# Performance work log

Measured on AMD Instinct MI355X. Metric: run time of the kernel, lower is better.

Reference implementation:

```python
import jax, jax.numpy as jnp
import numpy as np

H = 16  # hidden size

def _lstm_scan(xproj, Whh, bhh, collect_outputs):
    # xproj: [T, B, 4H] = input projection (W_ih @ x + b_ih), PyTorch gate order i,f,g,o
    B = xproj.shape[1]
    h0 = jnp.zeros((B, H), xproj.dtype)
    c0 = jnp.zeros((B, H), xproj.dtype)

    def step(carry, xt):
        h, c = carry
        g = xt + h @ Whh.T + bhh                      # [B, 4H]
        i, f, gg, o = jnp.split(g, 4, axis=-1)
        i = jax.nn.sigmoid(i)
        f = jax.nn.sigmoid(f)
        gg = jnp.tanh(gg)
        o = jax.nn.sigmoid(o)
        c = f * c + i * gg
        h = o * jnp.tanh(c)
        return (h, c), (h if collect_outputs else None)

    (hT, cT), hs = jax.lax.scan(step, (h0, c0), xproj)
    return hT, hs  # hs: [T, B, H] or None


def setup_inputs() -> dict:
    key = jax.random.key(0)
    ks = jax.random.split(key, 12)
    B, T = 4096, 1024
    s = 1.0 / np.sqrt(H)  # PyTorch LSTM init scale
    inp = {
        "x": jax.random.normal(ks[0], (B, T, 1), jnp.float32),
        "Wih0": jax.random.uniform(ks[1], (4 * H, 1), jnp.float32, -s, s),
        "Whh0": jax.random.uniform(ks[2], (4 * H, H), jnp.float32, -s, s),
        "bih0": jax.random.uniform(ks[3], (4 * H,), jnp.float32, -s, s),
        "bhh0": jax.random.uniform(ks[4], (4 * H,), jnp.float32, -s, s),
        "Wih1": jax.random.uniform(ks[5], (4 * H, H), jnp.float32, -s, s),
        "Whh1": jax.random.uniform(ks[6], (4 * H, H), jnp.float32, -s, s),
        "bih1": jax.random.uniform(ks[7], (4 * H,), jnp.float32, -s, s),
        "bhh1": jax.random.uniform(ks[8], (4 * H,), jnp.float32, -s, s),
        "Wout": jax.random.uniform(ks[9], (5, H), jnp.float32, -s, s),
        "bout": jax.random.uniform(ks[10], (5,), jnp.float32, -s, s),
    }
    return inp


def reference(x, Wih0, Whh0, bih0, bhh0, Wih1, Whh1, bih1, bhh1, Wout, bout):
    # Layer 1: precompute input projection for all timesteps, scan recurrence.
    # x: [B, T, 1] -> [T, B, 4H]
    xp0 = jnp.transpose(x @ Wih0.T + bih0, (1, 0, 2))
    _, hs1 = _lstm_scan(xp0, Whh0, bhh0, collect_outputs=True)  # [T, B, H]
    # Layer 2 (eval mode: dropout between layers is identity); only final h needed.
    xp1 = hs1 @ Wih1.T + bih1                                   # [T, B, 4H]
    hT, _ = _lstm_scan(xp1, Whh1, bhh1, collect_outputs=False)  # [B, H]
    # Head: ReLU then Linear(16 -> 5)
    return jax.nn.relu(hT) @ Wout.T + bout
```

## Files before the change

### kernel.cpp

```cpp
#include <hip/hip_runtime.h>

static constexpr int T_LEN = 1024;

typedef _Float16 f16;
typedef f16  f16x4 __attribute__((ext_vector_type(4)));
typedef float f32x4 __attribute__((ext_vector_type(4)));

__device__ __forceinline__ f32x4 mfma16(f16x4 a, f16x4 b, f32x4 c) {
    return __builtin_amdgcn_mfma_f32_16x16x16f16(a, b, c, 0, 0, 0);
}
__device__ __forceinline__ float sig2(float t) {
    return __builtin_amdgcn_rcpf(1.f + __builtin_amdgcn_exp2f(t));
}

__global__ void __launch_bounds__(512, 1) lstm2_xlds_kernel(
    const float* __restrict__ x,
    const float* __restrict__ Wih0, const float* __restrict__ Whh0,
    const float* __restrict__ bih0, const float* __restrict__ bhh0,
    const float* __restrict__ Wih1, const float* __restrict__ Whh1,
    const float* __restrict__ bih1, const float* __restrict__ bhh1,
    const float* __restrict__ Wout, const float* __restrict__ bout,
    float* __restrict__ out)
{
    const int tid = threadIdx.x;
    const int w8  = tid >> 6;
    const int lyr = w8 >> 2;
    const int q   = w8 & 3;
    const int l   = tid & 63;
    const int n   = l & 15;
    const int Lq  = l >> 4;
    const int seq = blockIdx.x * 16 + n;

    __shared__ __align__(16) f16   x_lds[16][1028];
    __shared__ __align__(16) f16   hx[2][16][36];
    __shared__ __align__(16) float h2fin[16][20];

    {
        const float* xblk = x + (size_t)blockIdx.x * 16 * T_LEN;
#pragma unroll
        for (int jj = 0; jj < 8; ++jj) {
            const int flat = jj * 2048 + tid * 4;
            const int row  = flat >> 10, col = flat & 1023;
            const float4 v = *reinterpret_cast<const float4*>(xblk + (size_t)row * T_LEN + col);
            f16x4 h4; h4[0] = (f16)v.x; h4[1] = (f16)v.y;
                      h4[2] = (f16)v.z; h4[3] = (f16)v.w;
            *reinterpret_cast<f16x4*>(&x_lds[row][col]) = h4;
        }
    }

    const float L2E = 1.442695041f;
    const float NT  = -2.f * L2E;

    const int   gA    = n & 3;
    const int   wrowA = gA * 16 + 4 * q + (n >> 2);
    const float nsA   = (gA == 2) ? (-2.f * L2E) : (-L2E);
    const int   u1    = 4 * q + Lq;

    f16x4 WaA = {}, WaB = {};
    f32x4 cbD, wxD = {};
#pragma unroll
    for (int r = 0; r < 4; ++r) {
        const float nsD  = (r == 2) ? (-2.f * L2E) : (-L2E);
        const int   wrdD = r * 16 + u1;
        if (lyr == 0) {
            WaA[r] = (f16)(nsA * Whh0[wrowA * 16 + 4 * Lq + r]);
            cbD[r] = nsD * (bih0[wrdD] + bhh0[wrdD]);
            wxD[r] = nsD * Wih0[wrdD];
        } else {
            WaA[r] = (f16)(nsA * Wih1[wrowA * 16 + 4 * Lq + r]);
            WaB[r] = (f16)(nsA * Whh1[wrowA * 16 + 4 * Lq + r]);
            cbD[r] = nsD * (bih1[wrdD] + bhh1[wrdD]);
        }
    }
    asm volatile("" : "+v"(WaA), "+v"(WaB), "+v"(cbD), "+v"(wxD));

    f16x4 h1f = {}, h2f = {};
    float c1 = 0.f, c2 = 0.f;
    f32x4 pre2 = cbD;

    __syncthreads();

    f16x4 xq = {};
    if (lyr == 0) xq = *reinterpret_cast<const f16x4*>(&x_lds[n][0]);

    for (int tb = 0; tb < T_LEN; tb += 4) {
        f16x4 xn = xq;
        if (lyr == 0 && tb + 4 < T_LEN)
            xn = *reinterpret_cast<const f16x4*>(&x_lds[n][tb + 4]);
#pragma unroll
        for (int u = 0; u < 4; ++u) {
            const int   t    = tb + u;
            const int   slot = u & 1;

            if (lyr == 0) {
                const float xv = (float)xq[u];
                f32x4 ci;
#pragma unroll
                for (int r = 0; r < 4; ++r)
                    ci[r] = fmaf(wxD[r], xv, cbD[r]);
                const f32x4 d = mfma16(WaA, h1f, ci);
                const float si = sig2(d[0]);
                const float sf = sig2(d[1]);
                const float sg = fmaf(2.f, sig2(d[2]), -1.f);
                const float so = sig2(d[3]);
                c1 = fmaf(sf, c1, si * sg);
                const float th = fmaf(2.f, sig2(NT * c1), -1.f);
                hx[slot][n][u1] = (f16)(so * th);
            } else if (t >= 1) {
                const f32x4 d = mfma16(WaA, h1f, pre2);
                const float si = sig2(d[0]);
                const float sf = sig2(d[1]);
                const float sg = fmaf(2.f, sig2(d[2]), -1.f);
                const float so = sig2(d[3]);
                c2 = fmaf(sf, c2, si * sg);
                const float th = fmaf(2.f, sig2(NT * c2), -1.f);
                hx[slot][n][16 + u1] = (f16)(so * th);
            }
            __syncthreads();

            h1f = *reinterpret_cast<const f16x4*>(&hx[slot][n][4 * Lq]);
            if (lyr == 1 && t >= 1) {
                h2f = *reinterpret_cast<const f16x4*>(&hx[slot][n][16 + 4 * Lq]);
                pre2 = mfma16(WaB, h2f, cbD);
            }
        }
        xq = xn;
    }

    if (lyr == 1) {
        const f32x4 d = mfma16(WaA, h1f, pre2);
        const float si = sig2(d[0]);
        const float sf = sig2(d[1]);
        const float sg = fmaf(2.f, sig2(d[2]), -1.f);
        const float so = sig2(d[3]);
        c2 = fmaf(sf, c2, si * sg);
        const float th = fmaf(2.f, sig2(NT * c2), -1.f);
        h2fin[n][u1] = so * th;
    }
    __syncthreads();

    if (w8 == 0) {
        const f32x4 hv = *reinterpret_cast<const f32x4*>(&h2fin[n][4 * Lq]);
#pragma unroll
        for (int m5 = 0; m5 < 5; ++m5) {
            float p = 0.f;
#pragma unroll
            for (int r = 0; r < 4; ++r)
                p = fmaf(fmaxf(hv[r], 0.f), Wout[m5 * 16 + 4 * Lq + r], p);
            p += __shfl_xor(p, 16, 64);
            p += __shfl_xor(p, 32, 64);
            if (Lq == 0) out[seq * 5 + m5] = p + bout[m5];
        }
    }
}

extern "C" void kernel_launch(void* const* d_in, const int* in_sizes, int n_in,
                              void* d_out, int out_size, void* d_ws, size_t ws_size,
                              hipStream_t stream) {
    const float* x    = (const float*)d_in[0];
    const float* Wih0 = (const float*)d_in[1];
    const float* Whh0 = (const float*)d_in[2];
    const float* bih0 = (const float*)d_in[3];
    const float* bhh0 = (const float*)d_in[4];
    const float* Wih1 = (const float*)d_in[5];
    const float* Whh1 = (const float*)d_in[6];
    const float* bih1 = (const float*)d_in[7];
    const float* bhh1 = (const float*)d_in[8];
    const float* Wout = (const float*)d_in[9];
    const float* bout = (const float*)d_in[10];
    float* out = (float*)d_out;

    const int B = in_sizes[0] / T_LEN;
    dim3 grid(B / 16), block(512);
    hipLaunchKernelGGL(lstm2_xlds_kernel, grid, block, 0, stream,
                       x, Wih0, Whh0, bih0, bhh0,
                       Wih1, Whh1, bih1, bhh1, Wout, bout, out);
}
```

Before: 253.8 us.

## Replace per-step block barriers with LDS flag-tagged polling between waves

Each hidden-state element is now written to LDS as a 32-bit word holding the timestep tag in the high half and the f16 value in the low half. Consumer waves spin on the four words they need instead of waiting at a __syncthreads after every timestep. An 8-slot ring buffer lets layers run ahead of each other, with a full barrier only every fourth step. The goal is to remove the per-step block-wide barrier cost, at the price of volatile LDS polling traffic and reliance on LDS write ordering between waves.

```diff
diff --git a/kernel.cpp b/kernel.cpp
--- a/kernel.cpp
+++ b/kernel.cpp
@@ -5,6 +5,7 @@
 typedef _Float16 f16;
 typedef f16  f16x4 __attribute__((ext_vector_type(4)));
 typedef float f32x4 __attribute__((ext_vector_type(4)));
+typedef unsigned int u32;
 
 __device__ __forceinline__ f32x4 mfma16(f16x4 a, f16x4 b, f32x4 c) {
     return __builtin_amdgcn_mfma_f32_16x16x16f16(a, b, c, 0, 0, 0);
@@ -12,8 +13,25 @@
 __device__ __forceinline__ float sig2(float t) {
     return __builtin_amdgcn_rcpf(1.f + __builtin_amdgcn_exp2f(t));
 }
-
-__global__ void __launch_bounds__(512, 1) lstm2_xlds_kernel(
+__device__ __forceinline__ u32 h16bits(float v) {
+    union { f16 h; unsigned short b; } cv;
+    cv.h = (f16)v;
+    return (u32)cv.b;
+}
+__device__ __forceinline__ f16x4 pollq(volatile const u32* vp, u32 want) {
+    u32 a, b, c, d;
+    for (;;) {
+        a = vp[0]; b = vp[1]; c = vp[2]; d = vp[3];
+        if ((((a ^ want) | (b ^ want) | (c ^ want) | (d ^ want)) >> 16) == 0)
+            break;
+    }
+    union { u32 u[2]; f16x4 h; } cv;
+    cv.u[0] = (a & 0xFFFFu) | (b << 16);
+    cv.u[1] = (c & 0xFFFFu) | (d << 16);
+    return cv.h;
+}
+
+__global__ void __launch_bounds__(512, 1) lstm2_flag_kernel(
     const float* __restrict__ x,
     const float* __restrict__ Wih0, const float* __restrict__ Whh0,
     const float* __restrict__ bih0, const float* __restrict__ bhh0,
@@ -32,8 +50,14 @@
     const int seq = blockIdx.x * 16 + n;
 
     __shared__ __align__(16) f16   x_lds[16][1028];
-    __shared__ __align__(16) f16   hx[2][16][36];
+    __shared__ u32 sync[8][2][4][16][4];
     __shared__ __align__(16) float h2fin[16][20];
+
+    {
+        u32* s = &sync[0][0][0][0][0];
+#pragma unroll
+        for (int i = 0; i < 8; ++i) s[tid + i * 512] = 0;
+    }
 
     {
         const float* xblk = x + (size_t)blockIdx.x * 16 * T_LEN;
@@ -89,10 +113,11 @@
             xn = *reinterpret_cast<const f16x4*>(&x_lds[n][tb + 4]);
 #pragma unroll
         for (int u = 0; u < 4; ++u) {
-            const int   t    = tb + u;
-            const int   slot = u & 1;
+            const int t = tb + u;
 
             if (lyr == 0) {
+                const int slot = t & 7;
+                const u32 want = (u32)(t + 1) << 16;
                 const float xv = (float)xq[u];
                 f32x4 ci;
 #pragma unroll
@@ -105,8 +130,13 @@
                 const float so = sig2(d[3]);
                 c1 = fmaf(sf, c1, si * sg);
                 const float th = fmaf(2.f, sig2(NT * c1), -1.f);
-                hx[slot][n][u1] = (f16)(so * th);
+                ((volatile u32*)&sync[slot][0][q][n][Lq])[0]
+                    = want | h16bits(so * th);
+                h1f = pollq(&sync[slot][0][Lq][n][0], want);
             } else if (t >= 1) {
+                const int slot = (t - 1) & 7;
+                const u32 want = (u32)t << 16;
+                h1f = pollq(&sync[slot][0][Lq][n][0], want);
                 const f32x4 d = mfma16(WaA, h1f, pre2);
                 const float si = sig2(d[0]);
                 const float sf = sig2(d[1]);
@@ -114,20 +144,19 @@
                 const float so = sig2(d[3]);
                 c2 = fmaf(sf, c2, si * sg);
                 const float th = fmaf(2.f, sig2(NT * c2), -1.f);
-                hx[slot][n][16 + u1] = (f16)(so * th);
-            }
-            __syncthreads();
-
-            h1f = *reinterpret_cast<const f16x4*>(&hx[slot][n][4 * Lq]);
-            if (lyr == 1 && t >= 1) {
-                h2f = *reinterpret_cast<const f16x4*>(&hx[slot][n][16 + 4 * Lq]);
+                ((volatile u32*)&sync[slot][1][q][n][Lq])[0]
+                    = want | h16bits(so * th);
+                h2f = pollq(&sync[slot][1][Lq][n][0], want);
                 pre2 = mfma16(WaB, h2f, cbD);
             }
+            if ((t & 3) == 3) __syncthreads();
         }
         xq = xn;
     }
 
     if (lyr == 1) {
+        const u32 want = (u32)T_LEN << 16;
+        h1f = pollq(&sync[(T_LEN - 1) & 7][0][Lq][n][0], want);
         const f32x4 d = mfma16(WaA, h1f, pre2);
         const float si = sig2(d[0]);
         const float sf = sig2(d[1]);
@@ -172,7 +201,7 @@
 
     const int B = in_sizes[0] / T_LEN;
     dim3 grid(B / 16), block(512);
-    hipLaunchKernelGGL(lstm2_xlds_kernel, grid, block, 0, stream,
+    hipLaunchKernelGGL(lstm2_flag_kernel, grid, block, 0, stream,
                        x, Wih0, Whh0, bih0, bhh0,
                        Wih1, Whh1, bih1, bhh1, Wout, bout, out);
 }
```

New measurement: 553.9 us. 118% more time.

## Fuse both LSTM layers into each wave with one-step skew, halve block size

Applied to the files above, without the earlier changes.

Instead of dedicating four waves to layer 0 and four to layer 1, each of four waves now computes a layer-0 step and the lagged layer-1 step in the same iteration, sharing one barrier per step. This aims to reduce barrier cost and expose instruction-level parallelism between the two independent layer computations. In exchange each SIMD holds only one wave, so MFMA and transcendental latency can no longer be hidden by a second wave, and per-wave serial work roughly doubles. Two epilogue steps finish the layer-1 recurrence.

```diff
diff --git a/kernel.cpp b/kernel.cpp
--- a/kernel.cpp
+++ b/kernel.cpp
@@ -13,7 +13,7 @@
     return __builtin_amdgcn_rcpf(1.f + __builtin_amdgcn_exp2f(t));
 }
 
-__global__ void __launch_bounds__(512, 1) lstm2_xlds_kernel(
+__global__ void __launch_bounds__(256, 1) lstm2_fw_kernel(
     const float* __restrict__ x,
     const float* __restrict__ Wih0, const float* __restrict__ Whh0,
     const float* __restrict__ bih0, const float* __restrict__ bhh0,
@@ -23,25 +23,24 @@
     float* __restrict__ out)
 {
     const int tid = threadIdx.x;
-    const int w8  = tid >> 6;
-    const int lyr = w8 >> 2;
-    const int q   = w8 & 3;
+    const int q   = tid >> 6;
     const int l   = tid & 63;
     const int n   = l & 15;
     const int Lq  = l >> 4;
     const int seq = blockIdx.x * 16 + n;
 
     __shared__ __align__(16) f16   x_lds[16][1028];
-    __shared__ __align__(16) f16   hx[2][16][36];
+    __shared__ __align__(16) f16   hx[2][2][16][20];
     __shared__ __align__(16) float h2fin[16][20];
 
     {
         const float* xblk = x + (size_t)blockIdx.x * 16 * T_LEN;
-#pragma unroll
-        for (int jj = 0; jj < 8; ++jj) {
-            const int flat = jj * 2048 + tid * 4;
+#pragma unroll 4
+        for (int jj = 0; jj < 16; ++jj) {
+            const int flat = jj * 1024 + tid * 4;
             const int row  = flat >> 10, col = flat & 1023;
-            const float4 v = *reinterpret_cast<const float4*>(xblk + (size_t)row * T_LEN + col);
+            const float4 v = *reinterpret_cast<const float4*>(
+                xblk + (size_t)row * T_LEN + col);
             f16x4 h4; h4[0] = (f16)v.x; h4[1] = (f16)v.y;
                       h4[2] = (f16)v.z; h4[3] = (f16)v.w;
             *reinterpret_cast<f16x4*>(&x_lds[row][col]) = h4;
@@ -56,90 +55,108 @@
     const float nsA   = (gA == 2) ? (-2.f * L2E) : (-L2E);
     const int   u1    = 4 * q + Lq;
 
-    f16x4 WaA = {}, WaB = {};
-    f32x4 cbD, wxD = {};
+    f16x4 WA, WAx, WB;
+    f32x4 cb1, wx0, cb2;
 #pragma unroll
     for (int r = 0; r < 4; ++r) {
         const float nsD  = (r == 2) ? (-2.f * L2E) : (-L2E);
         const int   wrdD = r * 16 + u1;
-        if (lyr == 0) {
-            WaA[r] = (f16)(nsA * Whh0[wrowA * 16 + 4 * Lq + r]);
-            cbD[r] = nsD * (bih0[wrdD] + bhh0[wrdD]);
-            wxD[r] = nsD * Wih0[wrdD];
-        } else {
-            WaA[r] = (f16)(nsA * Wih1[wrowA * 16 + 4 * Lq + r]);
-            WaB[r] = (f16)(nsA * Whh1[wrowA * 16 + 4 * Lq + r]);
-            cbD[r] = nsD * (bih1[wrdD] + bhh1[wrdD]);
-        }
+        WA[r]  = (f16)(nsA * Whh0[wrowA * 16 + 4 * Lq + r]);
+        WAx[r] = (f16)(nsA * Wih1[wrowA * 16 + 4 * Lq + r]);
+        WB[r]  = (f16)(nsA * Whh1[wrowA * 16 + 4 * Lq + r]);
+        cb1[r] = nsD * (bih0[wrdD] + bhh0[wrdD]);
+        wx0[r] = nsD * Wih0[wrdD];
+        cb2[r] = nsD * (bih1[wrdD] + bhh1[wrdD]);
     }
-    asm volatile("" : "+v"(WaA), "+v"(WaB), "+v"(cbD), "+v"(wxD));
+    asm volatile("" : "+v"(WA), "+v"(WAx), "+v"(WB),
+                      "+v"(cb1), "+v"(wx0), "+v"(cb2));
 
-    f16x4 h1f = {}, h2f = {};
+    f16x4 rh1 = {};
+    f16x4 h1A = {};
+    f16x4 rh2 = {};
+    f32x4 pre2;
     float c1 = 0.f, c2 = 0.f;
-    f32x4 pre2 = cbD;
+    f32x4 h2w = {0.f, 0.f, 0.f, 0.f};
 
     __syncthreads();
 
-    f16x4 xq = {};
-    if (lyr == 0) xq = *reinterpret_cast<const f16x4*>(&x_lds[n][0]);
+    f16x4 xq = *reinterpret_cast<const f16x4*>(&x_lds[n][0]);
 
     for (int tb = 0; tb < T_LEN; tb += 4) {
         f16x4 xn = xq;
-        if (lyr == 0 && tb + 4 < T_LEN)
+        if (tb + 4 < T_LEN)
             xn = *reinterpret_cast<const f16x4*>(&x_lds[n][tb + 4]);
 #pragma unroll
         for (int u = 0; u < 4; ++u) {
-            const int   t    = tb + u;
-            const int   slot = u & 1;
+            const int t    = tb + u;
+            const int slot = u & 1;
 
-            if (lyr == 0) {
+            if (t >= 2) {
+                const f32x4 p2 = mfma16(WB, rh2, cb2);
+                const f32x4 d2 = mfma16(WAx, h1A, p2);
+                const float si = sig2(d2[0]);
+                const float sf = sig2(d2[1]);
+                const float sg = fmaf(2.f, sig2(d2[2]), -1.f);
+                const float so = sig2(d2[3]);
+                c2 = fmaf(sf, c2, si * sg);
+                const float th = fmaf(2.f, sig2(NT * c2), -1.f);
+                hx[slot][1][n][u1] = (f16)(so * th);
+            }
+
+            {
                 const float xv = (float)xq[u];
                 f32x4 ci;
 #pragma unroll
                 for (int r = 0; r < 4; ++r)
-                    ci[r] = fmaf(wxD[r], xv, cbD[r]);
-                const f32x4 d = mfma16(WaA, h1f, ci);
-                const float si = sig2(d[0]);
-                const float sf = sig2(d[1]);
-                const float sg = fmaf(2.f, sig2(d[2]), -1.f);
-                const float so = sig2(d[3]);
+                    ci[r] = fmaf(wx0[r], xv, cb1[r]);
+                const f32x4 d1 = mfma16(WA, rh1, ci);
+                const float si = sig2(d1[0]);
+                const float sf = sig2(d1[1]);
+                const float sg = fmaf(2.f, sig2(d1[2]), -1.f);
+                const float so = sig2(d1[3]);
                 c1 = fmaf(sf, c1, si * sg);
                 const float th = fmaf(2.f, sig2(NT * c1), -1.f);
-                hx[slot][n][u1] = (f16)(so * th);
-            } else if (t >= 1) {
-                const f32x4 d = mfma16(WaA, h1f, pre2);
-                const float si = sig2(d[0]);
-                const float sf = sig2(d[1]);
-                const float sg = fmaf(2.f, sig2(d[2]), -1.f);
-                const float so = sig2(d[3]);
-                c2 = fmaf(sf, c2, si * sg);
-                const float th = fmaf(2.f, sig2(NT * c2), -1.f);
-                hx[slot][n][16 + u1] = (f16)(so * th);
+                hx[slot][0][n][u1] = (f16)(so * th);
             }
             __syncthreads();
 
-            h1f = *reinterpret_cast<const f16x4*>(&hx[slot][n][4 * Lq]);
-            if (lyr == 1 && t >= 1) {
-                h2f = *reinterpret_cast<const f16x4*>(&hx[slot][n][16 + 4 * Lq]);
-                pre2 = mfma16(WaB, h2f, cbD);
-            }
+            h1A = rh1;
+            rh1 = *reinterpret_cast<const f16x4*>(&hx[slot][0][n][4 * Lq]);
+            if (t >= 2)
+                rh2 = *reinterpret_cast<const f16x4*>(&hx[slot][1][n][4 * Lq]);
         }
         xq = xn;
     }
 
-    if (lyr == 1) {
-        const f32x4 d = mfma16(WaA, h1f, pre2);
-        const float si = sig2(d[0]);
-        const float sf = sig2(d[1]);
-        const float sg = fmaf(2.f, sig2(d[2]), -1.f);
-        const float so = sig2(d[3]);
+    float h2fv;
+    {
+        const f32x4 p2 = mfma16(WB, rh2, cb2);
+        const f32x4 d2 = mfma16(WAx, h1A, p2);
+        const float si = sig2(d2[0]);
+        const float sf = sig2(d2[1]);
+        const float sg = fmaf(2.f, sig2(d2[2]), -1.f);
+        const float so = sig2(d2[3]);
         c2 = fmaf(sf, c2, si * sg);
         const float th = fmaf(2.f, sig2(NT * c2), -1.f);
-        h2fin[n][u1] = so * th;
+        hx[0][1][n][u1] = (f16)(so * th);
+    }
+    __syncthreads();
+    {
+        const f16x4 h2x = *reinterpret_cast<const f16x4*>(&hx[0][1][n][4 * Lq]);
+        const f32x4 p2 = mfma16(WB, h2x, cb2);
+        const f32x4 d2 = mfma16(WAx, rh1, p2);
+        const float si = sig2(d2[0]);
+        const float sf = sig2(d2[1]);
+        const float sg = fmaf(2.f, sig2(d2[2]), -1.f);
+        const float so = sig2(d2[3]);
+        c2 = fmaf(sf, c2, si * sg);
+        const float th = fmaf(2.f, sig2(NT * c2), -1.f);
+        h2fv = so * th;
+        h2fin[n][u1] = h2fv;
     }
     __syncthreads();
 
-    if (w8 == 0) {
+    if (q == 0) {
         const f32x4 hv = *reinterpret_cast<const f32x4*>(&h2fin[n][4 * Lq]);
 #pragma unroll
         for (int m5 = 0; m5 < 5; ++m5) {
@@ -171,8 +188,8 @@
     float* out = (float*)d_out;
 
     const int B = in_sizes[0] / T_LEN;
-    dim3 grid(B / 16), block(512);
-    hipLaunchKernelGGL(lstm2_xlds_kernel, grid, block, 0, stream,
+    dim3 grid(B / 16), block(256);
+    hipLaunchKernelGGL(lstm2_fw_kernel, grid, block, 0, stream,
                        x, Wih0, Whh0, bih0, bhh0,
                        Wih1, Whh1, bih1, bhh1, Wout, bout, out);
 }
```

Result: slower. 274.4 us (+8.1%).

## Merge both LSTM layers into one K=32 MFMA per wave per step

Applied to the files above, without the earlier changes.

Replaces the split design (4 waves per layer, each running a 16x16x16 MFMA, with layer 2 issuing a second MFMA for its recurrent term) with a single 16x16x32 MFMA per wave. That MFMA's block-diagonal weight matrix covers layer-1 recurrence and layer-2 input plus recurrence together over the concatenated [h1,h2] vector. Each wave now computes 2 hidden units of both layers, which removes the extra dependent MFMA and one LDS read from the layer-2 path within each barrier step. The cost is a padded K dimension (zeros for the layer-1 rows) and a t==0 masking branch for layer 2.

```diff
diff --git a/kernel.cpp b/kernel.cpp
--- a/kernel.cpp
+++ b/kernel.cpp
@@ -4,16 +4,17 @@
 
 typedef _Float16 f16;
 typedef f16  f16x4 __attribute__((ext_vector_type(4)));
+typedef f16  f16x8 __attribute__((ext_vector_type(8)));
 typedef float f32x4 __attribute__((ext_vector_type(4)));
 
-__device__ __forceinline__ f32x4 mfma16(f16x4 a, f16x4 b, f32x4 c) {
-    return __builtin_amdgcn_mfma_f32_16x16x16f16(a, b, c, 0, 0, 0);
+__device__ __forceinline__ f32x4 mfma_k32(f16x8 a, f16x8 b, f32x4 c) {
+    return __builtin_amdgcn_mfma_f32_16x16x32_f16(a, b, c, 0, 0, 0);
 }
 __device__ __forceinline__ float sig2(float t) {
     return __builtin_amdgcn_rcpf(1.f + __builtin_amdgcn_exp2f(t));
 }
 
-__global__ void __launch_bounds__(512, 1) lstm2_xlds_kernel(
+__global__ void __launch_bounds__(512, 1) lstm2_k32_kernel(
     const float* __restrict__ x,
     const float* __restrict__ Wih0, const float* __restrict__ Whh0,
     const float* __restrict__ bih0, const float* __restrict__ bhh0,
@@ -22,14 +23,14 @@
     const float* __restrict__ Wout, const float* __restrict__ bout,
     float* __restrict__ out)
 {
-    const int tid = threadIdx.x;
-    const int w8  = tid >> 6;
-    const int lyr = w8 >> 2;
-    const int q   = w8 & 3;
-    const int l   = tid & 63;
-    const int n   = l & 15;
-    const int Lq  = l >> 4;
-    const int seq = blockIdx.x * 16 + n;
+    const int tid  = threadIdx.x;
+    const int w    = tid >> 6;
+    const int l    = tid & 63;
+    const int n    = l & 15;
+    const int Lq   = l >> 4;
+    const int isL2 = Lq >> 1;
+    const int u2   = 2 * w + (Lq & 1);
+    const int seq  = blockIdx.x * 16 + n;
 
     __shared__ __align__(16) f16   x_lds[16][1028];
     __shared__ __align__(16) f16   hx[2][16][36];
@@ -41,7 +42,8 @@
         for (int jj = 0; jj < 8; ++jj) {
             const int flat = jj * 2048 + tid * 4;
             const int row  = flat >> 10, col = flat & 1023;
-            const float4 v = *reinterpret_cast<const float4*>(xblk + (size_t)row * T_LEN + col);
+            const float4 v = *reinterpret_cast<const float4*>(
+                xblk + (size_t)row * T_LEN + col);
             f16x4 h4; h4[0] = (f16)v.x; h4[1] = (f16)v.y;
                       h4[2] = (f16)v.z; h4[3] = (f16)v.w;
             *reinterpret_cast<f16x4*>(&x_lds[row][col]) = h4;
@@ -51,102 +53,95 @@
     const float L2E = 1.442695041f;
     const float NT  = -2.f * L2E;
 
-    const int   gA    = n & 3;
-    const int   wrowA = gA * 16 + 4 * q + (n >> 2);
-    const float nsA   = (gA == 2) ? (-2.f * L2E) : (-L2E);
-    const int   u1    = 4 * q + Lq;
-
-    f16x4 WaA = {}, WaB = {};
-    f32x4 cbD, wxD = {};
+    const int   mh  = n >> 2, mg = n & 3;
+    const float nsm = (mg == 2) ? (-2.f * L2E) : (-L2E);
+    f16x8 WA;
+#pragma unroll
+    for (int j = 0; j < 8; ++j) {
+        const int k = 8 * Lq + j;
+        float wv;
+        if (mh < 2) {
+            const int wr = mg * 16 + 2 * w + mh;
+            wv = (k < 16) ? Whh0[wr * 16 + k] : 0.f;
+        } else {
+            const int wr = mg * 16 + 2 * w + (mh - 2);
+            wv = (k < 16) ? Wih1[wr * 16 + k] : Whh1[wr * 16 + (k - 16)];
+        }
+        WA[j] = (f16)(nsm * wv);
+    }
+    f32x4 cbD, wxD;
 #pragma unroll
     for (int r = 0; r < 4; ++r) {
-        const float nsD  = (r == 2) ? (-2.f * L2E) : (-L2E);
-        const int   wrdD = r * 16 + u1;
-        if (lyr == 0) {
-            WaA[r] = (f16)(nsA * Whh0[wrowA * 16 + 4 * Lq + r]);
-            cbD[r] = nsD * (bih0[wrdD] + bhh0[wrdD]);
-            wxD[r] = nsD * Wih0[wrdD];
+        const float nsD = (r == 2) ? (-2.f * L2E) : (-L2E);
+        const int   row = r * 16 + u2;
+        if (!isL2) {
+            cbD[r] = nsD * (bih0[row] + bhh0[row]);
+            wxD[r] = nsD * Wih0[row];
         } else {
-            WaA[r] = (f16)(nsA * Wih1[wrowA * 16 + 4 * Lq + r]);
-            WaB[r] = (f16)(nsA * Whh1[wrowA * 16 + 4 * Lq + r]);
-            cbD[r] = nsD * (bih1[wrdD] + bhh1[wrdD]);
+            cbD[r] = nsD * (bih1[row] + bhh1[row]);
+            wxD[r] = 0.f;
         }
     }
-    asm volatile("" : "+v"(WaA), "+v"(WaB), "+v"(cbD), "+v"(wxD));
+    asm volatile("" : "+v"(WA), "+v"(cbD), "+v"(wxD));
 
-    f16x4 h1f = {}, h2f = {};
-    float c1 = 0.f, c2 = 0.f;
-    f32x4 pre2 = cbD;
+    f16x8 rh = {};
+    float cc = 0.f;
 
     __syncthreads();
 
-    f16x4 xq = {};
-    if (lyr == 0) xq = *reinterpret_cast<const f16x4*>(&x_lds[n][0]);
+    f16x4 xq = *reinterpret_cast<const f16x4*>(&x_lds[n][0]);
 
     for (int tb = 0; tb < T_LEN; tb += 4) {
         f16x4 xn = xq;
-        if (lyr == 0 && tb + 4 < T_LEN)
+        if (tb + 4 < T_LEN)
             xn = *reinterpret_cast<const f16x4*>(&x_lds[n][tb + 4]);
 #pragma unroll
         for (int u = 0; u < 4; ++u) {
-            const int   t    = tb + u;
-            const int   slot = u & 1;
+            const int t    = tb + u;
+            const int slot = u & 1;
 
-            if (lyr == 0) {
-                const float xv = (float)xq[u];
-                f32x4 ci;
+            const float xv = (float)xq[u];
+            f32x4 ci;
 #pragma unroll
-                for (int r = 0; r < 4; ++r)
-                    ci[r] = fmaf(wxD[r], xv, cbD[r]);
-                const f32x4 d = mfma16(WaA, h1f, ci);
-                const float si = sig2(d[0]);
-                const float sf = sig2(d[1]);
-                const float sg = fmaf(2.f, sig2(d[2]), -1.f);
-                const float so = sig2(d[3]);
-                c1 = fmaf(sf, c1, si * sg);
-                const float th = fmaf(2.f, sig2(NT * c1), -1.f);
-                hx[slot][n][u1] = (f16)(so * th);
-            } else if (t >= 1) {
-                const f32x4 d = mfma16(WaA, h1f, pre2);
-                const float si = sig2(d[0]);
-                const float sf = sig2(d[1]);
-                const float sg = fmaf(2.f, sig2(d[2]), -1.f);
-                const float so = sig2(d[3]);
-                c2 = fmaf(sf, c2, si * sg);
-                const float th = fmaf(2.f, sig2(NT * c2), -1.f);
-                hx[slot][n][16 + u1] = (f16)(so * th);
-            }
+            for (int r = 0; r < 4; ++r)
+                ci[r] = fmaf(wxD[r], xv, cbD[r]);
+            const f32x4 d = mfma_k32(WA, rh, ci);
+            const float si = sig2(d[0]);
+            const float sf = sig2(d[1]);
+            const float sg = fmaf(2.f, sig2(d[2]), -1.f);
+            const float so = sig2(d[3]);
+            float ccn = fmaf(sf, cc, si * sg);
+            const float th = fmaf(2.f, sig2(NT * ccn), -1.f);
+            float hv = so * th;
+            if (t == 0 && isL2) { ccn = 0.f; hv = 0.f; }
+            cc = ccn;
+            hx[slot][n][isL2 * 16 + u2] = (f16)hv;
             __syncthreads();
-
-            h1f = *reinterpret_cast<const f16x4*>(&hx[slot][n][4 * Lq]);
-            if (lyr == 1 && t >= 1) {
-                h2f = *reinterpret_cast<const f16x4*>(&hx[slot][n][16 + 4 * Lq]);
-                pre2 = mfma16(WaB, h2f, cbD);
-            }
+            rh = *reinterpret_cast<const f16x8*>(&hx[slot][n][8 * Lq]);
         }
         xq = xn;
     }
 
-    if (lyr == 1) {
-        const f32x4 d = mfma16(WaA, h1f, pre2);
+    {
+        const f32x4 d = mfma_k32(WA, rh, cbD);
         const float si = sig2(d[0]);
         const float sf = sig2(d[1]);
         const float sg = fmaf(2.f, sig2(d[2]), -1.f);
         const float so = sig2(d[3]);
-        c2 = fmaf(sf, c2, si * sg);
-        const float th = fmaf(2.f, sig2(NT * c2), -1.f);
-        h2fin[n][u1] = so * th;
+        const float c2f = fmaf(sf, cc, si * sg);
+        const float th  = fmaf(2.f, sig2(NT * c2f), -1.f);
+        if (isL2) h2fin[n][u2] = so * th;
     }
     __syncthreads();
 
-    if (w8 == 0) {
-        const f32x4 hv = *reinterpret_cast<const f32x4*>(&h2fin[n][4 * Lq]);
+    if (w == 0) {
+        const f32x4 hv4 = *reinterpret_cast<const f32x4*>(&h2fin[n][4 * Lq]);
 #pragma unroll
         for (int m5 = 0; m5 < 5; ++m5) {
             float p = 0.f;
 #pragma unroll
             for (int r = 0; r < 4; ++r)
-                p = fmaf(fmaxf(hv[r], 0.f), Wout[m5 * 16 + 4 * Lq + r], p);
+                p = fmaf(fmaxf(hv4[r], 0.f), Wout[m5 * 16 + 4 * Lq + r], p);
             p += __shfl_xor(p, 16, 64);
             p += __shfl_xor(p, 32, 64);
             if (Lq == 0) out[seq * 5 + m5] = p + bout[m5];
@@ -172,7 +167,7 @@
 
     const int B = in_sizes[0] / T_LEN;
     dim3 grid(B / 16), block(512);
-    hipLaunchKernelGGL(lstm2_xlds_kernel, grid, block, 0, stream,
+    hipLaunchKernelGGL(lstm2_k32_kernel, grid, block, 0, stream,
                        x, Wih0, Whh0, bih0, bhh0,
                        Wih1, Whh1, bih1, bhh1, Wout, bout, out);
 }
```

Result: faster. 243.3 us (-4.1%).
